# Kernel optimization log

Measured on AMD Instinct MI355X. Metric: run time of the kernel, lower is better.

Reference implementation:

```python
import math
import jax, jax.numpy as jnp
import numpy as np

DN = ('NCHW', 'OIHW', 'NCHW')

def _conv2d(x, w, b, stride, padding='VALID'):
    y = jax.lax.conv_general_dilated(x, w, window_strides=stride, padding=padding,
                                     dimension_numbers=DN)
    return y + b[None, :, None, None]

def _same_padding_conv(x, w, b, s):
    # replicate torch same_padding_conv: ceil-mode SAME padding, then VALID conv
    H, W = x.shape[2], x.shape[3]
    kh, kw = w.shape[2], w.shape[3]
    out_h, out_w = math.ceil(H / s[0]), math.ceil(W / s[1])
    pad_h = max((out_h - 1) * s[0] + kh - H, 0)
    pad_w = max((out_w - 1) * s[1] + kw - W, 0)
    pt, pl = pad_h // 2, pad_w // 2
    x = jnp.pad(x, ((0, 0), (0, 0), (pt, pad_h - pt), (pl, pad_w - pl)))
    return _conv2d(x, w, b, s)

def _leaky(x):
    return jax.nn.leaky_relu(x, negative_slope=0.2)

def setup_inputs() -> dict:
    key = jax.random.key(0)
    ks = jax.random.split(key, 8)
    B, cin, cout, H, W = 2, 16, 24, 384, 1280
    fl = jax.random.normal(ks[0], (B, cin, H, W), jnp.float32)
    fr = jax.random.normal(ks[1], (B, cin, H, W), jnp.float32)
    w_em = jax.random.normal(ks[2], (cout, cin, 4, 4), jnp.float32) * 0.05
    b_em = jax.random.normal(ks[3], (cout,), jnp.float32) * 0.05
    w_rc = jax.random.normal(ks[4], (cout, cout, 1, 1), jnp.float32) * 0.1
    b_rc = jax.random.normal(ks[5], (cout,), jnp.float32) * 0.05
    w_tf = jax.random.normal(ks[6], (13, cout + 1, 1, 1), jnp.float32) * 0.1
    b_tf = jax.random.normal(ks[7], (13,), jnp.float32) * 0.05
    return {'feature_left': fl, 'feature_right': fr, 'max_disp': 64,
            'w_em': w_em, 'b_em': b_em, 'w_rc': w_rc, 'b_rc': b_rc,
            'w_tf': w_tf, 'b_tf': b_tf}

def reference(feature_left, feature_right, max_disp, w_em, b_em, w_rc, b_rc, w_tf, b_tf):
    # left branch: 4x4 conv, stride (4,4), VALID (torch default padding=0)
    fl = _leaky(_conv2d(_leaky(_conv2d(feature_left, w_em, b_em, (4, 4))), w_rc, b_rc, (1, 1)))
    # right branch: same-padding conv with stride (4,1) -> full width retained
    fr = _leaky(_conv2d(_leaky(_same_padding_conv(feature_right, w_em, b_em, (4, 1))), w_rc, b_rc, (1, 1)))
    B, C, Hq, Wq = fl.shape
    Wr = fr.shape[3]
    # clipped gather indices: idx[d, x] = clip(4*x - d + 1, 0, Wr-1)
    d = jnp.arange(max_disp)[:, None]          # [D,1]
    x = jnp.arange(Wq)[None, :]                # [1,Wq]
    idx = jnp.clip(4 * x - d + 1, 0, Wr - 1)   # [D,Wq]
    fr_g = jnp.take(fr, idx, axis=3)           # [B,C,H,D,Wq]
    # L1 cost over channels -> [B,D,H,Wq]
    cost_volume = jnp.sum(jnp.abs(fl[:, :, :, None, :] - fr_g), axis=1).transpose(0, 2, 1, 3)
    cost_f = jnp.min(cost_volume, axis=1, keepdims=True)                  # [B,1,H,Wq]
    d_init = jnp.argmin(cost_volume, axis=1, keepdims=True).astype(fl.dtype)
    p_init = jnp.concatenate([cost_f, fl], axis=1)
    p_init = _leaky(_conv2d(p_init, w_tf, b_tf, (1, 1)))                  # [B,13,H,Wq]
    z = jnp.zeros_like(d_init)
    out = jnp.concatenate([d_init, z, z, p_init], axis=1)                 # [B,16,H,Wq]
    return out, cost_volume
```

## Files before the change

kernel.cpp:

```cpp
#include <hip/hip_runtime.h>

#define B_   2
#define CIN  16
#define HIN  384
#define WIN  1280
#define CO   24
#define HQ   96
#define WL   320
#define WR   1280
#define DMAX 64

__device__ __forceinline__ float lk(float v) { return v >= 0.f ? v : 0.2f * v; }

__global__ __launch_bounds__(256) void k_em(
    const float* __restrict__ xl, const float* __restrict__ xr,
    const float* __restrict__ w_em, const float* __restrict__ b_em,
    const float* __restrict__ w_rc, const float* __restrict__ b_rc,
    float* __restrict__ out_l, float* __restrict__ out_r)
{
    __shared__ __align__(16) float buf[CO * CIN * 16];
    __shared__ __align__(16) float swt[CO * CO];
    __shared__ float sbe[CO], sbr[CO];

    for (int i = threadIdx.x; i < CO * CIN * 16; i += 256) buf[i] = w_em[i];
    for (int i = threadIdx.x; i < CO * CO; i += 256) swt[i] = w_rc[(i % CO) * CO + (i / CO)];
    if (threadIdx.x < CO) { sbe[threadIdx.x] = b_em[threadIdx.x]; sbr[threadIdx.x] = b_rc[threadIdx.x]; }
    __syncthreads();

    const int t = threadIdx.x;

    if (blockIdx.x < 960) {
        const int rb = blockIdx.x;
        const int L = t & 63, quarter = t >> 6;
        const int obase = quarter * 6;
        const int row = rb / 5, jbase = (rb % 5) * 256;
        const int b = row / HQ, h = row % HQ;

        const bool vm1 = (jbase + 4 * L) > 0;
        const bool vp  = (jbase + 4 * L + 4) < WIN;
        const int  om1 = vm1 ? (4 * L - 2) : 0;
        const int  op4 = vp  ? (4 * L + 4) : 0;

        float acc[4][6];
#pragma unroll
        for (int k = 0; k < 4; ++k)
#pragma unroll
            for (int oo = 0; oo < 6; ++oo) acc[k][oo] = sbe[obase + oo];

        for (int c = 0; c < CIN; ++c) {
#pragma unroll
            for (int kh = 0; kh < 4; ++kh) {
                const float* xp = xr + ((size_t)(b * CIN + c) * HIN + 4 * h + kh) * WIN + jbase;
                const float4  v = *(const float4*)(xp + 4 * L);
                const float2  A = *(const float2*)(xp + om1);
                const float2  C = *(const float2*)(xp + op4);
                float in[7];
                in[0] = vm1 ? A.y : 0.f;
                in[1] = v.x; in[2] = v.y; in[3] = v.z; in[4] = v.w;
                in[5] = vp ? C.x : 0.f;
                in[6] = vp ? C.y : 0.f;
#pragma unroll
                for (int oo = 0; oo < 6; ++oo) {
                    const float4 wv = *(const float4*)&buf[(((obase + oo) * CIN + c) * 4 + kh) * 4];
#pragma unroll
                    for (int k = 0; k < 4; ++k) {
                        float a = acc[k][oo];
                        a = fmaf(in[k],     wv.x, a);
                        a = fmaf(in[k + 1], wv.y, a);
                        a = fmaf(in[k + 2], wv.z, a);
                        a = fmaf(in[k + 3], wv.w, a);
                        acc[k][oo] = a;
                    }
                }
            }
        }
        __syncthreads();
#pragma unroll
        for (int oo = 0; oo < 6; ++oo) {
            float4 st = make_float4(lk(acc[0][oo]), lk(acc[1][oo]), lk(acc[2][oo]), lk(acc[3][oo]));
            *(float4*)&buf[(obase + oo) * 256 + 4 * L] = st;
        }
        __syncthreads();

        float acc2[CO];
#pragma unroll
        for (int o = 0; o < CO; ++o) acc2[o] = sbr[o];
        for (int c = 0; c < CO; ++c) {
            const float in_c = buf[c * 256 + t];
#pragma unroll
            for (int m = 0; m < 6; ++m) {
                const float4 wv = *(const float4*)&swt[c * CO + 4 * m];
                acc2[4 * m + 0] = fmaf(in_c, wv.x, acc2[4 * m + 0]);
                acc2[4 * m + 1] = fmaf(in_c, wv.y, acc2[4 * m + 1]);
                acc2[4 * m + 2] = fmaf(in_c, wv.z, acc2[4 * m + 2]);
                acc2[4 * m + 3] = fmaf(in_c, wv.w, acc2[4 * m + 3]);
            }
        }
#pragma unroll
        for (int o = 0; o < CO; ++o)
            out_r[((size_t)(b * CO + o) * HQ + h) * WR + jbase + t] = lk(acc2[o]);
    } else {
        const int lb = blockIdx.x - 960;
        const int half = t >> 7, pxl = t & 127;
        const int obase = half * 12;
        const int flat = lb * 128 + pxl;
        const int j = flat % WL, h = (flat / WL) % HQ, b = flat / (WL * HQ);

        float acc[12];
#pragma unroll
        for (int oo = 0; oo < 12; ++oo) acc[oo] = sbe[obase + oo];

        for (int c = 0; c < CIN; ++c) {
#pragma unroll
            for (int kh = 0; kh < 4; ++kh) {
                const float4 v = *(const float4*)(xl + ((size_t)(b * CIN + c) * HIN + 4 * h + kh) * WIN + 4 * j);
#pragma unroll
                for (int oo = 0; oo < 12; ++oo) {
                    const float4 wv = *(const float4*)&buf[(((obase + oo) * CIN + c) * 4 + kh) * 4];
                    acc[oo] += v.x * wv.x + v.y * wv.y + v.z * wv.z + v.w * wv.w;
                }
            }
        }
        __syncthreads();
#pragma unroll
        for (int oo = 0; oo < 12; ++oo) buf[(obase + oo) * 128 + pxl] = lk(acc[oo]);
        __syncthreads();

        float acc2[12];
#pragma unroll
        for (int oo = 0; oo < 12; ++oo) acc2[oo] = sbr[obase + oo];
        for (int c = 0; c < CO; ++c) {
            const float in_c = buf[c * 128 + pxl];
#pragma unroll
            for (int oo = 0; oo < 12; ++oo) acc2[oo] += in_c * swt[c * CO + obase + oo];
        }
#pragma unroll
        for (int oo = 0; oo < 12; ++oo)
            out_l[((size_t)(b * CO + obase + oo) * HQ + h) * WL + j] = lk(acc2[oo]);
    }
}

__global__ __launch_bounds__(256) void k_cost(
    const float* __restrict__ fl, const float* __restrict__ fr,
    const float* __restrict__ wtf, const float* __restrict__ btf,
    float* __restrict__ out, float* __restrict__ cost)
{
    __shared__ float frs[CO * 324];
    __shared__ float sbest[256];
    __shared__ int   sbd[256];

    const int t  = threadIdx.x;
    const int j  = t & 63;
    const int w  = t >> 6;
    const int jc = blockIdx.x % 5;
    const int r  = blockIdx.x / 5;
    const int h  = r % HQ, b = r / HQ;
    const int j0 = jc * 64;
    const int jg = j0 + j;
    const int colbase = 4 * j0 - 64;

    for (int idx = t; idx < CO * 320; idx += 256) {
        const int c = idx / 320, Wd = idx % 320;
        const int col = colbase + Wd;
        frs[c * 324 + 2 + Wd] = fr[((size_t)(b * CO + c) * HQ + h) * WR + (col > 0 ? col : 0)];
    }
    __syncthreads();

    float acc[4][4];
#pragma unroll
    for (int q = 0; q < 4; ++q)
#pragma unroll
        for (int rr = 0; rr < 4; ++rr) acc[q][rr] = 0.f;

    for (int c = 0; c < CO; ++c) {
        const float flc = fl[((size_t)(b * CO + c) * HQ + h) * WL + jg];
        const float* base = &frs[c * 324 + 4 * j + 64];
#pragma unroll
        for (int q = 0; q < 4; ++q) {
            const int D = 4 * w + q;
            const float4 v = *(const float4*)(base - 4 * D);
            acc[q][0] += fabsf(flc - v.w);
            acc[q][1] += fabsf(flc - v.z);
            acc[q][2] += fabsf(flc - v.y);
            acc[q][3] += fabsf(flc - v.x);
        }
    }

#pragma unroll
    for (int q = 0; q < 4; ++q)
#pragma unroll
        for (int rr = 0; rr < 4; ++rr) {
            const int d = 16 * w + 4 * q + rr;
            cost[((size_t)(b * DMAX + d) * HQ + h) * WL + jg] = acc[q][rr];
        }

    float best = acc[0][0]; int bd = 16 * w;
#pragma unroll
    for (int q = 0; q < 4; ++q)
#pragma unroll
        for (int rr = 0; rr < 4; ++rr) {
            if (q == 0 && rr == 0) continue;
            const int d = 16 * w + 4 * q + rr;
            if (acc[q][rr] < best) { best = acc[q][rr]; bd = d; }
        }
    sbest[t] = best; sbd[t] = bd;
    __syncthreads();

    float cur = sbest[j]; int curd = sbd[j];
#pragma unroll
    for (int g = 1; g < 4; ++g) {
        const float v = sbest[g * 64 + j];
        if (v < cur) { cur = v; curd = sbd[g * 64 + j]; }
    }
    float flr[CO];
#pragma unroll
    for (int c = 0; c < CO; ++c) flr[c] = fl[((size_t)(b * CO + c) * HQ + h) * WL + jg];

    const int o_lo = (w == 0) ? 0 : 4 * w - 3;
    const int o_hi = 4 * w + 1;
    for (int o = o_lo; o < o_hi; ++o) {
        float a = btf[o] + wtf[o * 25] * cur;
#pragma unroll
        for (int c = 0; c < CO; ++c) a += wtf[o * 25 + 1 + c] * flr[c];
        out[((size_t)(b * 16 + 3 + o) * HQ + h) * WL + jg] = lk(a);
    }
    if (w == 0) {
        out[((size_t)(b * 16 + 0) * HQ + h) * WL + jg] = (float)curd;
        out[((size_t)(b * 16 + 1) * HQ + h) * WL + jg] = 0.f;
        out[((size_t)(b * 16 + 2) * HQ + h) * WL + jg] = 0.f;
    }
}

extern "C" void kernel_launch(void* const* d_in, const int* in_sizes, int n_in,
                              void* d_out, int out_size, void* d_ws, size_t ws_size,
                              hipStream_t stream) {
    const float* fl_in = (const float*)d_in[0];
    const float* fr_in = (const float*)d_in[1];
    const float* w_em = (const float*)d_in[3];
    const float* b_em = (const float*)d_in[4];
    const float* w_rc = (const float*)d_in[5];
    const float* b_rc = (const float*)d_in[6];
    const float* w_tf = (const float*)d_in[7];
    const float* b_tf = (const float*)d_in[8];

    float* out  = (float*)d_out;
    float* cost = out + (size_t)B_ * 16 * HQ * WL;

    float* fl_ws = (float*)d_ws;
    float* fr_ws = fl_ws + (size_t)B_ * CO * HQ * WL;

    hipLaunchKernelGGL(k_em, dim3(1440), dim3(256), 0, stream,
                       fl_in, fr_in, w_em, b_em, w_rc, b_rc, fl_ws, fr_ws);
    hipLaunchKernelGGL(k_cost, dim3(960), dim3(256), 0, stream,
                       fl_ws, fr_ws, w_tf, b_tf, out, cost);
}
```

Measured before the change: 231.3 us.

## Merge left and right embedding branches into uniform blocks sharing weight loads

Removes the split where 960 blocks handled the right branch and 480 blocks handled the left. Now every one of 960 blocks computes a right-branch tile plus 64 left-branch pixels. Each left pixel is computed by four thread groups, each owning 6 output channels, and the loop reuses the same shared-memory weight loads for both branches. The aim is to balance the work per block, drop the divergent branch, and share weight reads, at the cost of more registers per thread and an extra shared buffer for the left activations.

```diff
diff --git a/kernel.cpp b/kernel.cpp
--- a/kernel.cpp
+++ b/kernel.cpp
@@ -19,6 +19,7 @@
     float* __restrict__ out_l, float* __restrict__ out_r)
 {
     __shared__ __align__(16) float buf[CO * CIN * 16];
+    __shared__ __align__(16) float lacts[CO * 64];
     __shared__ __align__(16) float swt[CO * CO];
     __shared__ float sbe[CO], sbr[CO];
 
@@ -28,116 +29,102 @@
     __syncthreads();
 
     const int t = threadIdx.x;
-
-    if (blockIdx.x < 960) {
-        const int rb = blockIdx.x;
-        const int L = t & 63, quarter = t >> 6;
-        const int obase = quarter * 6;
-        const int row = rb / 5, jbase = (rb % 5) * 256;
-        const int b = row / HQ, h = row % HQ;
-
-        const bool vm1 = (jbase + 4 * L) > 0;
-        const bool vp  = (jbase + 4 * L + 4) < WIN;
-        const int  om1 = vm1 ? (4 * L - 2) : 0;
-        const int  op4 = vp  ? (4 * L + 4) : 0;
-
-        float acc[4][6];
-#pragma unroll
-        for (int k = 0; k < 4; ++k)
-#pragma unroll
-            for (int oo = 0; oo < 6; ++oo) acc[k][oo] = sbe[obase + oo];
-
-        for (int c = 0; c < CIN; ++c) {
-#pragma unroll
-            for (int kh = 0; kh < 4; ++kh) {
-                const float* xp = xr + ((size_t)(b * CIN + c) * HIN + 4 * h + kh) * WIN + jbase;
-                const float4  v = *(const float4*)(xp + 4 * L);
-                const float2  A = *(const float2*)(xp + om1);
-                const float2  C = *(const float2*)(xp + op4);
-                float in[7];
-                in[0] = vm1 ? A.y : 0.f;
-                in[1] = v.x; in[2] = v.y; in[3] = v.z; in[4] = v.w;
-                in[5] = vp ? C.x : 0.f;
-                in[6] = vp ? C.y : 0.f;
-#pragma unroll
-                for (int oo = 0; oo < 6; ++oo) {
-                    const float4 wv = *(const float4*)&buf[(((obase + oo) * CIN + c) * 4 + kh) * 4];
-#pragma unroll
-                    for (int k = 0; k < 4; ++k) {
-                        float a = acc[k][oo];
-                        a = fmaf(in[k],     wv.x, a);
-                        a = fmaf(in[k + 1], wv.y, a);
-                        a = fmaf(in[k + 2], wv.z, a);
-                        a = fmaf(in[k + 3], wv.w, a);
-                        acc[k][oo] = a;
-                    }
+    const int L = t & 63, quarter = t >> 6;
+    const int obase = quarter * 6;
+    const size_t cstride = (size_t)HIN * WIN;
+
+    const int row = blockIdx.x / 5, jbase = (blockIdx.x % 5) * 256;
+    const int b = row / HQ, h = row % HQ;
+    const bool vm1 = (jbase + 4 * L) > 0;
+    const bool vp  = (jbase + 4 * L + 4) < WIN;
+    const int  om1 = vm1 ? (4 * L - 2) : 0;
+    const int  op4 = vp  ? (4 * L + 4) : 0;
+    const float* xrc = xr + ((size_t)(b * CIN) * HIN + 4 * h) * WIN + jbase;
+
+    const int lflat = blockIdx.x * 64 + L;
+    const int jL = lflat % WL, hL = (lflat / WL) % HQ, bL = lflat / (WL * HQ);
+    const float* xlc = xl + ((size_t)(bL * CIN) * HIN + 4 * hL) * WIN + 4 * jL;
+
+    float racc[4][6];
+    float lacc[6];
+#pragma unroll
+    for (int oo = 0; oo < 6; ++oo) {
+        const float be = sbe[obase + oo];
+#pragma unroll
+        for (int k = 0; k < 4; ++k) racc[k][oo] = be;
+        lacc[oo] = be;
+    }
+
+    for (int c = 0; c < CIN; ++c) {
+#pragma unroll
+        for (int kh = 0; kh < 4; ++kh) {
+            const float* xp = xrc + c * cstride + kh * WIN;
+            const float4  v = *(const float4*)(xp + 4 * L);
+            const float2  A = *(const float2*)(xp + om1);
+            const float2  C = *(const float2*)(xp + op4);
+            const float4 vl = *(const float4*)(xlc + c * cstride + kh * WIN);
+            float in[7];
+            in[0] = vm1 ? A.y : 0.f;
+            in[1] = v.x; in[2] = v.y; in[3] = v.z; in[4] = v.w;
+            in[5] = vp ? C.x : 0.f;
+            in[6] = vp ? C.y : 0.f;
+#pragma unroll
+            for (int oo = 0; oo < 6; ++oo) {
+                const float4 wv = *(const float4*)&buf[(((obase + oo) * CIN + c) * 4 + kh) * 4];
+#pragma unroll
+                for (int k = 0; k < 4; ++k) {
+                    float a = racc[k][oo];
+                    a = fmaf(in[k],     wv.x, a);
+                    a = fmaf(in[k + 1], wv.y, a);
+                    a = fmaf(in[k + 2], wv.z, a);
+                    a = fmaf(in[k + 3], wv.w, a);
+                    racc[k][oo] = a;
                 }
+                lacc[oo] += vl.x * wv.x + vl.y * wv.y + vl.z * wv.z + vl.w * wv.w;
             }
         }
-        __syncthreads();
-#pragma unroll
-        for (int oo = 0; oo < 6; ++oo) {
-            float4 st = make_float4(lk(acc[0][oo]), lk(acc[1][oo]), lk(acc[2][oo]), lk(acc[3][oo]));
-            *(float4*)&buf[(obase + oo) * 256 + 4 * L] = st;
-        }
-        __syncthreads();
-
-        float acc2[CO];
-#pragma unroll
-        for (int o = 0; o < CO; ++o) acc2[o] = sbr[o];
-        for (int c = 0; c < CO; ++c) {
-            const float in_c = buf[c * 256 + t];
-#pragma unroll
-            for (int m = 0; m < 6; ++m) {
-                const float4 wv = *(const float4*)&swt[c * CO + 4 * m];
-                acc2[4 * m + 0] = fmaf(in_c, wv.x, acc2[4 * m + 0]);
-                acc2[4 * m + 1] = fmaf(in_c, wv.y, acc2[4 * m + 1]);
-                acc2[4 * m + 2] = fmaf(in_c, wv.z, acc2[4 * m + 2]);
-                acc2[4 * m + 3] = fmaf(in_c, wv.w, acc2[4 * m + 3]);
-            }
-        }
-#pragma unroll
-        for (int o = 0; o < CO; ++o)
-            out_r[((size_t)(b * CO + o) * HQ + h) * WR + jbase + t] = lk(acc2[o]);
-    } else {
-        const int lb = blockIdx.x - 960;
-        const int half = t >> 7, pxl = t & 127;
-        const int obase = half * 12;
-        const int flat = lb * 128 + pxl;
-        const int j = flat % WL, h = (flat / WL) % HQ, b = flat / (WL * HQ);
-
-        float acc[12];
-#pragma unroll
-        for (int oo = 0; oo < 12; ++oo) acc[oo] = sbe[obase + oo];
-
-        for (int c = 0; c < CIN; ++c) {
-#pragma unroll
-            for (int kh = 0; kh < 4; ++kh) {
-                const float4 v = *(const float4*)(xl + ((size_t)(b * CIN + c) * HIN + 4 * h + kh) * WIN + 4 * j);
-#pragma unroll
-                for (int oo = 0; oo < 12; ++oo) {
-                    const float4 wv = *(const float4*)&buf[(((obase + oo) * CIN + c) * 4 + kh) * 4];
-                    acc[oo] += v.x * wv.x + v.y * wv.y + v.z * wv.z + v.w * wv.w;
-                }
-            }
-        }
-        __syncthreads();
-#pragma unroll
-        for (int oo = 0; oo < 12; ++oo) buf[(obase + oo) * 128 + pxl] = lk(acc[oo]);
-        __syncthreads();
-
-        float acc2[12];
-#pragma unroll
-        for (int oo = 0; oo < 12; ++oo) acc2[oo] = sbr[obase + oo];
-        for (int c = 0; c < CO; ++c) {
-            const float in_c = buf[c * 128 + pxl];
-#pragma unroll
-            for (int oo = 0; oo < 12; ++oo) acc2[oo] += in_c * swt[c * CO + obase + oo];
-        }
-#pragma unroll
-        for (int oo = 0; oo < 12; ++oo)
-            out_l[((size_t)(b * CO + obase + oo) * HQ + h) * WL + j] = lk(acc2[oo]);
-    }
+    }
+
+#pragma unroll
+    for (int oo = 0; oo < 6; ++oo) lacts[(obase + oo) * 64 + L] = lk(lacc[oo]);
+
+    __syncthreads();
+#pragma unroll
+    for (int oo = 0; oo < 6; ++oo) {
+        float4 st = make_float4(lk(racc[0][oo]), lk(racc[1][oo]), lk(racc[2][oo]), lk(racc[3][oo]));
+        *(float4*)&buf[(obase + oo) * 256 + 4 * L] = st;
+    }
+    __syncthreads();
+
+    float acc2[CO];
+#pragma unroll
+    for (int o = 0; o < CO; ++o) acc2[o] = sbr[o];
+    for (int c = 0; c < CO; ++c) {
+        const float in_c = buf[c * 256 + t];
+#pragma unroll
+        for (int m = 0; m < 6; ++m) {
+            const float4 wv = *(const float4*)&swt[c * CO + 4 * m];
+            acc2[4 * m + 0] = fmaf(in_c, wv.x, acc2[4 * m + 0]);
+            acc2[4 * m + 1] = fmaf(in_c, wv.y, acc2[4 * m + 1]);
+            acc2[4 * m + 2] = fmaf(in_c, wv.z, acc2[4 * m + 2]);
+            acc2[4 * m + 3] = fmaf(in_c, wv.w, acc2[4 * m + 3]);
+        }
+    }
+#pragma unroll
+    for (int o = 0; o < CO; ++o)
+        out_r[((size_t)(b * CO + o) * HQ + h) * WR + jbase + t] = lk(acc2[o]);
+
+    float acc2l[6];
+#pragma unroll
+    for (int oo = 0; oo < 6; ++oo) acc2l[oo] = sbr[obase + oo];
+    for (int c = 0; c < CO; ++c) {
+        const float in_c = lacts[c * 64 + L];
+#pragma unroll
+        for (int oo = 0; oo < 6; ++oo) acc2l[oo] += in_c * swt[c * CO + obase + oo];
+    }
+#pragma unroll
+    for (int oo = 0; oo < 6; ++oo)
+        out_l[((size_t)(bL * CO + obase + oo) * HQ + hL) * WL + jL] = lk(acc2l[oo]);
 }
 
 __global__ __launch_bounds__(256) void k_cost(
@@ -249,7 +236,7 @@
     float* fl_ws = (float*)d_ws;
     float* fr_ws = fl_ws + (size_t)B_ * CO * HQ * WL;
 
-    hipLaunchKernelGGL(k_em, dim3(1440), dim3(256), 0, stream,
+    hipLaunchKernelGGL(k_em, dim3(960), dim3(256), 0, stream,
                        fl_in, fr_in, w_em, b_em, w_rc, b_rc, fl_ws, fr_ws);
     hipLaunchKernelGGL(k_cost, dim3(960), dim3(256), 0, stream,
                        fl_ws, fr_ws, w_tf, b_tf, out, cost);
```

New measurement: 262.6 us. +13.5%, slower.
